# Optimization experiments

Hardware: AMD Instinct MI355X
Metric: run time of the kernel (lower is better)

## Reference

```python
import jax, jax.numpy as jnp
import numpy as np

B = 1024      # batch
HG = 28       # grid side (28x28 image -> graph)
N = HG * HG   # 784 nodes per sample
K = 70        # node_sampled (relaxed categorical classes)
GCN_OUT = 48
H_DIM = 400
Z = 70
IMG = 784
TEMP = 0.5


def _grid_edges():
    idx = np.arange(N).reshape(HG, HG)
    src = np.concatenate([idx[:, :-1].ravel(), idx[:, 1:].ravel(), idx[:-1, :].ravel(), idx[1:, :].ravel()])
    dst = np.concatenate([idx[:, 1:].ravel(), idx[:, :-1].ravel(), idx[1:, :].ravel(), idx[:-1, :].ravel()])
    loop = np.arange(N)
    return (np.concatenate([src, loop]).astype(np.int32),
            np.concatenate([dst, loop]).astype(np.int32))


def _lin(key, fi, fo):
    kw, kb = jax.random.split(key)
    s = 1.0 / np.sqrt(fi)
    return (jax.random.uniform(kw, (fi, fo), jnp.float32, -s, s),
            jax.random.uniform(kb, (fo,), jnp.float32, -s, s))


def setup_inputs() -> dict:
    key = jax.random.key(0)
    ks = jax.random.split(key, 16)
    src, dst = _grid_edges()
    u = jax.random.uniform(ks[2], (B, N, K), jnp.float32, 1e-6, 1.0 - 1e-6)
    inp = {
        'nodes': jax.random.normal(ks[0], (B, N, 2), jnp.float32),
        'logits': jax.random.normal(ks[1], (B, N, K), jnp.float32),
        'gumbel': -jnp.log(-jnp.log(u)),
        'eps': jax.random.normal(ks[3], (B, Z), jnp.float32),
    }
    inp['W1'], inp['b1'] = _lin(ks[4], 2, 16)
    inp['W2'], inp['b2'] = _lin(ks[5], 16, 32)
    inp['W3'], inp['b3'] = _lin(ks[6], 32, GCN_OUT)
    inp['We1'], inp['be1'] = _lin(ks[7], K * GCN_OUT, H_DIM)
    inp['We2'], inp['be2'] = _lin(ks[8], H_DIM, H_DIM)
    inp['Wmu'], inp['bmu'] = _lin(ks[9], H_DIM, Z)
    inp['Wvar'], inp['bvar'] = _lin(ks[10], H_DIM, Z)
    inp['Wd1'], inp['bd1'] = _lin(ks[11], Z, H_DIM)
    inp['Wd2'], inp['bd2'] = _lin(ks[12], H_DIM, IMG)
    inp['edge_src'] = jnp.asarray(src)
    inp['edge_dst'] = jnp.asarray(dst)
    return inp


def reference(nodes, logits, gumbel, eps,
              W1, b1, W2, b2, W3, b3,
              We1, be1, We2, be2,
              Wmu, bmu, Wvar, bvar,
              Wd1, bd1, Wd2, bd2,
              edge_src, edge_dst):
    # symmetric GCN normalization with self loops (already in edge list)
    deg = jnp.zeros((N,), nodes.dtype).at[edge_dst].add(1.0)
    dinv = jax.lax.rsqrt(deg)
    norm = dinv[edge_src] * dinv[edge_dst]  # [E]

    def gcn(h, W, b):
        h = h @ W                                   # [B,N,Fout]
        msg = h[:, edge_src] * norm[None, :, None]  # gather + scale, [B,E,Fout]
        return jnp.zeros_like(h).at[:, edge_dst].add(msg) + b

    h = jax.nn.relu(gcn(nodes, W1, b1))
    h = jax.nn.relu(gcn(h, W2, b2))
    h = jax.nn.relu(gcn(h, W3, b3))            # [B,N,48]

    # RelaxedOneHotCategorical(temp=0.5).rsample() == gumbel-softmax
    sample = jax.nn.softmax((logits + gumbel) / TEMP, axis=-1)  # [B,N,K]
    g = jnp.einsum('bnk,bnf->bkf', sample, h).reshape(h.shape[0], K * GCN_OUT)

    # encoder MLP + reparameterize
    e = jax.nn.relu(g @ We1 + be1)
    e = jax.nn.relu(e @ We2 + be2)
    mu = e @ Wmu + bmu
    var = jax.nn.softplus(e @ Wvar + bvar)
    z = mu + eps * jnp.sqrt(var + 1e-10)

    # decoder
    d = jax.nn.relu(z @ Wd1 + bd1)
    x_rec = jax.nn.sigmoid(d @ Wd2 + bd2)      # [B,784]
    return x_rec
```

## Files before the change

### kernel.cpp

```cpp
#include <hip/hip_runtime.h>
#include <hip/hip_bf16.h>


#define BB 1024
#define HG 28
#define NN 784
#define KK 70
#define F3 48
#define HD 400
#define ZD 70
#define IMGD 784

typedef __hip_bfloat16 bf16;
typedef __attribute__((ext_vector_type(8))) short s8v;
typedef __attribute__((ext_vector_type(4))) float f32x4;

__device__ __forceinline__ float dinv_ij(int i, int j){
  int deg = 1 + (i>0) + (i<HG-1) + (j>0) + (j<HG-1);
  return rsqrtf((float)deg);
}

__device__ __forceinline__ unsigned pk2(float a, float b){
  union { bf16 h; unsigned short u; } ua, ub;
  ua.h = __float2bfloat16(a); ub.h = __float2bfloat16(b);
  return ((unsigned)ub.u << 16) | ua.u;
}

__device__ __forceinline__ short bfbits(float v){
  union { bf16 h; short s; } u; u.h = __float2bfloat16(v); return u.s;
}

#define SYNC_LDS() do {                                   \
    asm volatile("" ::: "memory");                        \
    asm volatile("s_waitcnt lgkmcnt(0)" ::: "memory");    \
    __builtin_amdgcn_s_barrier();                         \
    asm volatile("" ::: "memory");                        \
  } while(0)

__global__ __launch_bounds__(256, 2)
void gcn_fused(const float* __restrict__ nodes,
               const float* __restrict__ W1, const float* __restrict__ b1,
               const float* __restrict__ W2, const float* __restrict__ b2,
               const float* __restrict__ W3, const float* __restrict__ b3,
               bf16* __restrict__ h3){
  __shared__ __align__(16) char smem[73216];
  float* regA = (float*)smem;
  float* regB = (float*)(smem + 36288);
  float* wbuf = (float*)(smem + 64512);
  float* W1s = wbuf;          float* b1s = wbuf + 32;
  float* W2s = wbuf + 48;     float* b2s = wbuf + 560;
  float* W3s = wbuf + 592;    float* b3s = wbuf + 2128;

  int tid = threadIdx.x;
  if (tid < 32)  W1s[tid] = W1[tid];
  if (tid < 16)  b1s[tid] = b1[tid];
  for (int t = tid; t < 512;  t += 256) W2s[t] = W2[t];
  if (tid < 32)  b2s[tid] = b2[tid];
  for (int t = tid; t < 1536; t += 256) W3s[t] = W3[t];
  if (tid < 48)  b3s[tid] = b3[tid];

  int b = blockIdx.x >> 2, s = blockIdx.x & 3;
  int base3 = s*7;
  int base2 = base3 - 1;
  int base1 = base3 - 2;
  const float* nb = nodes + (size_t)b*NN*2;
  __syncthreads();

  {
    float* h1s = regA;
    for (int t = tid; t < 308; t += 256){
      int lr = t/28, j = t - lr*28;
      int r = base1 + lr;
      float o[16] __attribute__((aligned(16)));
      if (r < 0 || r >= HG){
        #pragma unroll
        for (int f=0; f<16; f++) o[f] = 0.f;
      } else {
        float dn = dinv_ij(r,j);
        float a0 = dn*nb[(r*HG+j)*2+0], a1 = dn*nb[(r*HG+j)*2+1];
        if (r > 0)   { float w=dinv_ij(r-1,j); a0 += w*nb[((r-1)*HG+j)*2]; a1 += w*nb[((r-1)*HG+j)*2+1]; }
        if (r < HG-1){ float w=dinv_ij(r+1,j); a0 += w*nb[((r+1)*HG+j)*2]; a1 += w*nb[((r+1)*HG+j)*2+1]; }
        if (j > 0)   { float w=dinv_ij(r,j-1); a0 += w*nb[(r*HG+j-1)*2];   a1 += w*nb[(r*HG+j-1)*2+1]; }
        if (j < HG-1){ float w=dinv_ij(r,j+1); a0 += w*nb[(r*HG+j+1)*2];   a1 += w*nb[(r*HG+j+1)*2+1]; }
        a0 *= dn; a1 *= dn;
        #pragma unroll
        for (int f=0; f<16; f++) o[f] = fmaxf(a0*W1s[f] + a1*W1s[16+f] + b1s[f], 0.f);
      }
      float* dst = h1s + t*20;
      #pragma unroll
      for (int qq=0; qq<4; qq++) *(float4*)(dst + 4*qq) = *(float4*)&o[4*qq];
    }
  }
  __syncthreads();

  if (tid < 252){
    const float* h1s = regA;
    float* agg1 = regB;
    int lr = tid/28, j = tid - lr*28;
    int r = base2 + lr;
    float o[16] __attribute__((aligned(16)));
    if (r < 0 || r >= HG){
      #pragma unroll
      for (int f=0; f<16; f++) o[f] = 0.f;
    } else {
      int ln = (lr+1)*28 + j;
      float dn = dinv_ij(r,j);
      float wu = dinv_ij(r-1,j), wd = dinv_ij(r+1,j);
      float wl = (j>0)    ? dinv_ij(r,j-1) : 0.f;
      float wr = (j<HG-1) ? dinv_ij(r,j+1) : 0.f;
      const float* pc = h1s + ln*20;
      #pragma unroll
      for (int qq=0; qq<4; qq++){
        float4 vc = *(const float4*)(pc + 4*qq);
        float4 vu = *(const float4*)(pc - 28*20 + 4*qq);
        float4 vd = *(const float4*)(pc + 28*20 + 4*qq);
        float4 vl = *(const float4*)(pc - 20 + 4*qq);
        float4 vr = *(const float4*)(pc + 20 + 4*qq);
        o[4*qq+0] = dn*(dn*vc.x + wu*vu.x + wd*vd.x + wl*vl.x + wr*vr.x);
        o[4*qq+1] = dn*(dn*vc.y + wu*vu.y + wd*vd.y + wl*vl.y + wr*vr.y);
        o[4*qq+2] = dn*(dn*vc.z + wu*vu.z + wd*vd.z + wl*vl.z + wr*vr.z);
        o[4*qq+3] = dn*(dn*vc.w + wu*vu.w + wd*vd.w + wl*vl.w + wr*vr.w);
      }
    }
    float* dst = agg1 + tid*20;
    #pragma unroll
    for (int qq=0; qq<4; qq++) *(float4*)(dst + 4*qq) = *(float4*)&o[4*qq];
  }
  __syncthreads();

  {
    const float* agg1 = regB;
    float* h2s = regA;
    int tx = tid & 7, ty = tid >> 3;
    float4 w2r[16];
    #pragma unroll
    for (int fi=0; fi<16; fi++) w2r[fi] = *(const float4*)&W2s[fi*32 + tx*4];
    float4 bb = *(const float4*)&b2s[tx*4];
    #pragma unroll
    for (int i=0; i<8; i++){
      int n = ty + 32*i;
      if (n < 252){
        float af[16] __attribute__((aligned(16)));
        const float* ap = agg1 + n*20;
        #pragma unroll
        for (int qq=0; qq<4; qq++) *(float4*)&af[4*qq] = *(const float4*)(ap + 4*qq);
        float4 acc = bb;
        #pragma unroll
        for (int fi=0; fi<16; fi++){
          float a = af[fi];
          acc.x += a*w2r[fi].x; acc.y += a*w2r[fi].y;
          acc.z += a*w2r[fi].z; acc.w += a*w2r[fi].w;
        }
        acc.x = fmaxf(acc.x,0.f); acc.y = fmaxf(acc.y,0.f);
        acc.z = fmaxf(acc.z,0.f); acc.w = fmaxf(acc.w,0.f);
        *(float4*)&h2s[n*36 + tx*4] = acc;
      }
    }
  }
  __syncthreads();

  if (tid < 196){
    const float* h2s = regA;
    float* agg2 = regB;
    int lr = tid/28, j = tid - lr*28;
    int r = base3 + lr;
    int ln = (lr+1)*28 + j;
    float dn = dinv_ij(r,j);
    float wu = dinv_ij(r-1,j), wd = dinv_ij(r+1,j);
    float wl = (j>0)    ? dinv_ij(r,j-1) : 0.f;
    float wr = (j<HG-1) ? dinv_ij(r,j+1) : 0.f;
    const float* pc = h2s + ln*36;
    float* dst = agg2 + tid*36;
    #pragma unroll
    for (int qq=0; qq<8; qq++){
      float4 vc = *(const float4*)(pc + 4*qq);
      float4 vu = *(const float4*)(pc - 28*36 + 4*qq);
      float4 vd = *(const float4*)(pc + 28*36 + 4*qq);
      float4 vl = *(const float4*)(pc - 36 + 4*qq);
      float4 vr = *(const float4*)(pc + 36 + 4*qq);
      float4 o;
      o.x = dn*(dn*vc.x + wu*vu.x + wd*vd.x + wl*vl.x + wr*vr.x);
      o.y = dn*(dn*vc.y + wu*vu.y + wd*vd.y + wl*vl.y + wr*vr.y);
      o.z = dn*(dn*vc.z + wu*vu.z + wd*vd.z + wl*vl.z + wr*vr.z);
      o.w = dn*(dn*vc.w + wu*vu.w + wd*vd.w + wl*vl.w + wr*vr.w);
      *(float4*)(dst + 4*qq) = o;
    }
  }
  __syncthreads();

  {
    bf16* h3buf = (bf16*)regA;
    if (tid < 252){
      const float* agg2 = regB;
      int tx = tid % 12, ty = tid / 12;
      float4 w3r[32];
      #pragma unroll
      for (int fi=0; fi<32; fi++) w3r[fi] = *(const float4*)&W3s[fi*48 + tx*4];
      float4 bb = *(const float4*)&b3s[tx*4];
      #pragma unroll
      for (int i=0; i<10; i++){
        int n = ty + 21*i;
        if (n < 196){
          float af[32] __attribute__((aligned(16)));
          const float* ap = agg2 + n*36;
          #pragma unroll
          for (int qq=0; qq<8; qq++) *(float4*)&af[4*qq] = *(const float4*)(ap + 4*qq);
          float4 acc = bb;
          #pragma unroll
          for (int fi=0; fi<32; fi++){
            float a = af[fi];
            acc.x += a*w3r[fi].x; acc.y += a*w3r[fi].y;
            acc.z += a*w3r[fi].z; acc.w += a*w3r[fi].w;
          }
          uint2 pv;
          pv.x = pk2(fmaxf(acc.x,0.f), fmaxf(acc.y,0.f));
          pv.y = pk2(fmaxf(acc.z,0.f), fmaxf(acc.w,0.f));
          *(uint2*)((char*)h3buf + n*112 + tx*8) = pv;
        }
      }
    }
  }
  __syncthreads();

  {
    const char* h3buf = (const char*)regA;
    uint4* dst = (uint4*)(h3 + ((size_t)b*NN + base3*28)*F3);
    for (int t = tid; t < 1176; t += 256){
      int n = t/6, gq = t - n*6;
      dst[t] = *(const uint4*)(h3buf + n*112 + gq*16);
    }
  }
}

__global__ __launch_bounds__(256)
void einsum_mfma_kernel(const float* __restrict__ logits, const float* __restrict__ gumbel,
                        const bf16* __restrict__ h3, float* __restrict__ g){
  __shared__ __align__(16) unsigned smemD[2][7488];
  const int SLO = 2880, HTO = 5760;

  int b = blockIdx.x, tid = threadIdx.x;
  int l = tid & 63, w = tid >> 6;
  int n_loc = tid >> 2, q = tid & 3;
  int kstart = q << 4;
  int kcnt = (q < 3) ? 16 : 22;
  int kc2 = kcnt >> 1;
  int m_pair = tid >> 3;
  int half = (tid >> 2) & 1;
  int ks = w >> 1, mh = w & 1;
  int mtoff = mh ? 3 : 0, mtcnt = mh ? 2 : 3;

  for (int t = tid; t < 720; t += 256){
    int bb = t >= 360, r = t - bb*360;
    smemD[bb][2520 + r] = 0u;
    smemD[bb][SLO + 2520 + r] = 0u;
  }

  f32x4 acc[3][3];
  #pragma unroll
  for (int mt=0; mt<3; mt++)
    #pragma unroll
    for (int bt=0; bt<3; bt++) acc[mt][bt] = (f32x4){0.f,0.f,0.f,0.f};

  float2 lxA[11], gxA[11], lxB[11], gxB[11];
  uint2 hA0A, hB0A, hA1A, hB1A;
  uint2 hA0B, hB0B, hA1B, hB1B;
  int hm0 = tid/12, hj0 = tid - hm0*12;
  int tt1 = tid + 256;
  int hm1 = tt1/12, hj1 = tt1 - hm1*12;

  auto issue_into = [&](int c, float2 (&lx)[11], float2 (&gx)[11],
                        uint2& hA0, uint2& hB0, uint2& hA1, uint2& hB1){
    int c0 = c << 6;
    int node = c0 + n_loc;
    bool v = node < NN;
    const float* lp = logits + ((size_t)b*NN + node)*KK + kstart;
    const float* gp = gumbel + ((size_t)b*NN + node)*KK + kstart;
    int nld = (q < 3) ? 8 : 11;
    #pragma unroll
    for (int s=0; s<11; s++){
      bool a = v && (s < nld);
      lx[s] = a ? *(const float2*)(lp + 2*s) : (float2){0.f,0.f};
      gx[s] = a ? *(const float2*)(gp + 2*s) : (float2){0.f,0.f};
    }
    bool vA0 = (c0 + 2*hm0)     < NN;
    bool vB0 = (c0 + 2*hm0 + 1) < NN;
    const uint2* p0 = (const uint2*)(h3 + ((size_t)b*NN + c0 + 2*hm0)*F3 + 4*hj0);
    hA0 = vA0 ? p0[0]  : (uint2){0u,0u};
    hB0 = vB0 ? p0[12] : (uint2){0u,0u};
    if (tid < 128){
      bool vA1 = (c0 + 2*hm1)     < NN;
      bool vB1 = (c0 + 2*hm1 + 1) < NN;
      const uint2* p1 = (const uint2*)(h3 + ((size_t)b*NN + c0 + 2*hm1)*F3 + 4*hj1);
      hA1 = vA1 ? p1[0]  : (uint2){0u,0u};
      hB1 = vB1 ? p1[12] : (uint2){0u,0u};
    }
  };

  auto consume_from = [&](int c, unsigned* buf, float2 (&lx)[11], float2 (&gx)[11],
                          uint2& hA0, uint2& hB0, uint2& hA1, uint2& hB1){
    int c0 = c << 6;
    bool v = (c0 + n_loc) < NN;
    float x[22];
    #pragma unroll
    for (int s=0; s<11; s++){
      x[2*s]   = 2.f*(lx[s].x + gx[s].x);
      x[2*s+1] = 2.f*(lx[s].y + gx[s].y);
    }
    float mx = -1e30f;
    #pragma unroll
    for (int i=0; i<22; i++) if (i < kcnt) mx = fmaxf(mx, x[i]);
    mx = fmaxf(mx, __shfl_xor(mx, 1));
    mx = fmaxf(mx, __shfl_xor(mx, 2));
    float sum = 0.f;
    #pragma unroll
    for (int i=0; i<22; i++) if (i < kcnt){ x[i] = __expf(x[i]-mx); sum += x[i]; }
    sum += __shfl_xor(sum, 1);
    sum += __shfl_xor(sum, 2);
    float rs = v ? 1.0f/sum : 0.f;
    #pragma unroll
    for (int i=0; i<22; i++){
      if (i < kcnt){
        float p = x[i]*rs;
        unsigned hb = (unsigned)(unsigned short)bfbits(p);
        union { short s; bf16 h; } uh; uh.s = (short)hb;
        float lo = p - __bfloat162float(uh.h);
        unsigned lb = (unsigned)(unsigned short)bfbits(lo);
        unsigned phb = (unsigned)__shfl_xor((int)hb, 4);
        unsigned plb = (unsigned)__shfl_xor((int)lb, 4);
        unsigned dh = (half==0) ? (hb | (phb<<16)) : (phb | (hb<<16));
        unsigned dl = (half==0) ? (lb | (plb<<16)) : (plb | (lb<<16));
        bool doW = (half==0) ? (i < kc2) : (i >= kc2);
        if (doW){
          int k = kstart + i;
          int col = m_pair ^ (((k>>4)&3)<<3);
          buf[k*36 + col] = dh;
          buf[SLO + k*36 + col] = dl;
        }
      }
    }
    {
      unsigned d0 = (hA0.x & 0xFFFFu) | (hB0.x << 16);
      unsigned d1 = (hA0.x >> 16)     | (hB0.x & 0xFFFF0000u);
      unsigned d2 = (hA0.y & 0xFFFFu) | (hB0.y << 16);
      unsigned d3 = (hA0.y >> 16)     | (hB0.y & 0xFFFF0000u);
      #pragma unroll
      for (int i2=0; i2<4; i2++){
        int f = 4*hj0 + i2;
        int col = hm0 ^ (((f>>4)&3)<<3);
        unsigned dv = (i2==0)?d0:(i2==1)?d1:(i2==2)?d2:d3;
        buf[HTO + f*36 + col] = dv;
      }
      if (tid < 128){
        unsigned e0 = (hA1.x & 0xFFFFu) | (hB1.x << 16);
        unsigned e1 = (hA1.x >> 16)     | (hB1.x & 0xFFFF0000u);
        unsigned e2 = (hA1.y & 0xFFFFu) | (hB1.y << 16);
        unsigned e3 = (hA1.y >> 16)     | (hB1.y & 0xFFFF0000u);
        #pragma unroll
        for (int i2=0; i2<4; i2++){
          int f = 4*hj1 + i2;
          int col = hm1 ^ (((f>>4)&3)<<3);
          unsigned dv = (i2==0)?e0:(i2==1)?e1:(i2==2)?e2:e3;
          buf[HTO + f*36 + col] = dv;
        }
      }
    }
  };

  auto mfma_phase = [&](const unsigned* buf){
    int pr = (ks<<4) + ((l>>4)<<2);
    s8v Af[3], Al[3], Bf[3];
    #pragma unroll
    for (int mt=0; mt<3; mt++) if (mt < mtcnt){
      int row = (mtoff+mt)*16 + (l&15);
      int col = pr ^ (((row>>4)&3)<<3);
      Af[mt] = *(const s8v*)&buf[row*36 + col];
      Al[mt] = *(const s8v*)&buf[SLO + row*36 + col];
    }
    #pragma unroll
    for (int bt=0; bt<3; bt++){
      int f = bt*16 + (l&15);
      int col = pr ^ (((f>>4)&3)<<3);
      Bf[bt] = *(const s8v*)&buf[HTO + f*36 + col];
    }
    #pragma unroll
    for (int mt=0; mt<3; mt++) if (mt < mtcnt)
      #pragma unroll
      for (int bt=0; bt<3; bt++){
        acc[mt][bt] = __builtin_amdgcn_mfma_f32_16x16x32_bf16(Af[mt], Bf[bt], acc[mt][bt], 0, 0, 0);
        acc[mt][bt] = __builtin_amdgcn_mfma_f32_16x16x32_bf16(Al[mt], Bf[bt], acc[mt][bt], 0, 0, 0);
      }
  };

  issue_into(0, lxA, gxA, hA0A, hB0A, hA1A, hB1A);
  issue_into(1, lxB, gxB, hA0B, hB0B, hA1B, hB1B);
  consume_from(0, smemD[0], lxA, gxA, hA0A, hB0A, hA1A, hB1A);
  SYNC_LDS();

  for (int c = 0; c < 13; c++){
    if (c + 2 <= 12){
      if ((c & 1) == 0) issue_into(c+2, lxA, gxA, hA0A, hB0A, hA1A, hB1A);
      else              issue_into(c+2, lxB, gxB, hA0B, hB0B, hA1B, hB1B);
    }
    if (c < 12){
      if (((c+1) & 1) == 0) consume_from(c+1, smemD[(c+1)&1], lxA, gxA, hA0A, hB0A, hA1A, hB1A);
      else                  consume_from(c+1, smemD[(c+1)&1], lxB, gxB, hA0B, hB0B, hA1B, hB1B);
    }
    mfma_phase(smemD[c&1]);
    SYNC_LDS();
  }

  float* cred = (float*)&smemD[0][0];
  if (ks == 0){
    #pragma unroll
    for (int mt=0; mt<3; mt++) if (mt < mtcnt)
      #pragma unroll
      for (int bt=0; bt<3; bt++)
        #pragma unroll
        for (int r=0; r<4; r++){
          int row = (mtoff+mt)*16 + (l>>4)*4 + r;
          int col = bt*16 + (l&15);
          cred[row*49 + col] = acc[mt][bt][r];
        }
  }
  __syncthreads();
  if (ks == 1){
    #pragma unroll
    for (int mt=0; mt<3; mt++) if (mt < mtcnt)
      #pragma unroll
      for (int bt=0; bt<3; bt++)
        #pragma unroll
        for (int r=0; r<4; r++){
          int row = (mtoff+mt)*16 + (l>>4)*4 + r;
          int col = bt*16 + (l&15);
          cred[row*49 + col] += acc[mt][bt][r];
        }
  }
  __syncthreads();
  for (int t = tid; t < KK*F3; t += 256){
    int r = t / F3, c2 = t - r*F3;
    g[(size_t)b*(KK*F3) + t] = cred[r*49 + c2];
  }
}

template<int ACT>
__global__ __launch_bounds__(256)
void dense_kernel(const float* __restrict__ A, const float* __restrict__ W,
                  const float* __restrict__ bias, float* __restrict__ out,
                  int M, int K, int Nn, int kChunk){
  __shared__ float As[16][65];
  __shared__ float Bs[16][64];
  int tx = threadIdx.x & 15, ty = threadIdx.x >> 4;
  int m0 = blockIdx.x*64, n0 = blockIdx.y*64;
  int ks = blockIdx.z * kChunk;
  int ke = min(K, ks + kChunk);
  int a_kk = threadIdx.x & 15, a_mm = threadIdx.x >> 4;
  int b_nn = threadIdx.x & 63, b_k0 = threadIdx.x >> 6;
  float ra[4], rb[4];
  float acc[4][4] = {};

  #pragma unroll
  for (int s=0; s<4; s++){
    int gk = ks + a_kk;
    ra[s] = (gk < ke) ? A[(size_t)(m0 + a_mm + s*16)*K + gk] : 0.f;
  }
  #pragma unroll
  for (int s=0; s<4; s++){
    int gk = ks + b_k0 + s*4, gn = n0 + b_nn;
    rb[s] = (gk < ke && gn < Nn) ? W[(size_t)gk*Nn + gn] : 0.f;
  }

  for (int k0 = ks; k0 < ke; k0 += 16){
    #pragma unroll
    for (int s=0; s<4; s++) As[a_kk][a_mm + s*16] = ra[s];
    #pragma unroll
    for (int s=0; s<4; s++) Bs[b_k0 + s*4][b_nn] = rb[s];
    __syncthreads();
    if (k0 + 16 < ke){
      #pragma unroll
      for (int s=0; s<4; s++){
        int gk = k0 + 16 + a_kk;
        ra[s] = (gk < ke) ? A[(size_t)(m0 + a_mm + s*16)*K + gk] : 0.f;
      }
      #pragma unroll
      for (int s=0; s<4; s++){
        int gk = k0 + 16 + b_k0 + s*4, gn = n0 + b_nn;
        rb[s] = (gk < ke && gn < Nn) ? W[(size_t)gk*Nn + gn] : 0.f;
      }
    }
    #pragma unroll
    for (int kk=0; kk<16; kk++){
      float a[4], bv[4];
      #pragma unroll
      for (int i2=0; i2<4; i2++) a[i2] = As[kk][ty*4+i2];
      #pragma unroll
      for (int j2=0; j2<4; j2++) bv[j2] = Bs[kk][tx*4+j2];
      #pragma unroll
      for (int i2=0; i2<4; i2++)
        #pragma unroll
        for (int j2=0; j2<4; j2++) acc[i2][j2] += a[i2]*bv[j2];
    }
    __syncthreads();
  }

  if (ACT == 2){
    float* po = out + (size_t)blockIdx.z*M*Nn;
    #pragma unroll
    for (int j2=0; j2<4; j2++){
      int gn = n0 + tx*4 + j2;
      if (gn < Nn){
        #pragma unroll
        for (int i2=0; i2<4; i2++)
          po[(size_t)(m0 + ty*4 + i2)*Nn + gn] = acc[i2][j2];
      }
    }
  } else {
    #pragma unroll
    for (int j2=0; j2<4; j2++){
      int gn = n0 + tx*4 + j2;
      if (gn < Nn){
        float bb = bias[gn];
        #pragma unroll
        for (int i2=0; i2<4; i2++){
          float v = acc[i2][j2] + bb;
          v = (ACT == 0) ? fmaxf(v, 0.f) : 1.0f/(1.0f + __expf(-v));
          out[(size_t)(m0 + ty*4 + i2)*Nn + gn] = v;
        }
      }
    }
  }
}

__global__ __launch_bounds__(256)
void dense_dualB_partial(const float* __restrict__ A, const float* __restrict__ Wmu,
                         const float* __restrict__ Wvar, float* __restrict__ out,
                         int M, int K, int Nn, int kChunk){
  __shared__ float As[16][65];
  __shared__ float Bs[16][64];
  int tx = threadIdx.x & 15, ty = threadIdx.x >> 4;
  int m0 = blockIdx.x*64, n0 = blockIdx.y*64;
  int ks = blockIdx.z * kChunk;
  int ke = min(K, ks + kChunk);
  int a_kk = threadIdx.x & 15, a_mm = threadIdx.x >> 4;
  int b_nn = threadIdx.x & 63, b_k0 = threadIdx.x >> 6;
  float ra[4], rb[4];
  float acc[4][4] = {};

  auto bload = [&](int gk, int gn)->float{
    if (gk >= ke || gn >= Nn) return 0.f;
    return (gn < ZD) ? Wmu[(size_t)gk*ZD + gn] : Wvar[(size_t)gk*ZD + gn - ZD];
  };

  #pragma unroll
  for (int s=0; s<4; s++){
    int gk = ks + a_kk;
    ra[s] = (gk < ke) ? A[(size_t)(m0 + a_mm + s*16)*K + gk] : 0.f;
  }
  #pragma unroll
  for (int s=0; s<4; s++) rb[s] = bload(ks + b_k0 + s*4, n0 + b_nn);

  for (int k0 = ks; k0 < ke; k0 += 16){
    #pragma unroll
    for (int s=0; s<4; s++) As[a_kk][a_mm + s*16] = ra[s];
    #pragma unroll
    for (int s=0; s<4; s++) Bs[b_k0 + s*4][b_nn] = rb[s];
    __syncthreads();
    if (k0 + 16 < ke){
      #pragma unroll
      for (int s=0; s<4; s++){
        int gk = k0 + 16 + a_kk;
        ra[s] = (gk < ke) ? A[(size_t)(m0 + a_mm + s*16)*K + gk] : 0.f;
      }
      #pragma unroll
      for (int s=0; s<4; s++) rb[s] = bload(k0 + 16 + b_k0 + s*4, n0 + b_nn);
    }
    #pragma unroll
    for (int kk=0; kk<16; kk++){
      float a[4], bv[4];
      #pragma unroll
      for (int i2=0; i2<4; i2++) a[i2] = As[kk][ty*4+i2];
      #pragma unroll
      for (int j2=0; j2<4; j2++) bv[j2] = Bs[kk][tx*4+j2];
      #pragma unroll
      for (int i2=0; i2<4; i2++)
        #pragma unroll
        for (int j2=0; j2<4; j2++) acc[i2][j2] += a[i2]*bv[j2];
    }
    __syncthreads();
  }

  float* po = out + (size_t)blockIdx.z*M*Nn;
  #pragma unroll
  for (int j2=0; j2<4; j2++){
    int gn = n0 + tx*4 + j2;
    if (gn < Nn){
      #pragma unroll
      for (int i2=0; i2<4; i2++)
        po[(size_t)(m0 + ty*4 + i2)*Nn + gn] = acc[i2][j2];
    }
  }
}

template<int ACT>
__global__ __launch_bounds__(256)
void reduce_bias_act(const float* __restrict__ part, const float* __restrict__ bias,
                     float* __restrict__ out, int M, int Nn, int S){
  int idx = blockIdx.x*256 + threadIdx.x;
  if (idx >= M*Nn) return;
  int n = idx % Nn;
  float s = bias[n];
  for (int i=0; i<S; i++) s += part[(size_t)i*M*Nn + idx];
  out[idx] = (ACT == 0) ? fmaxf(s, 0.f) : 1.0f/(1.0f + __expf(-s));
}

__global__ __launch_bounds__(256)
void reduce_reparam(const float* __restrict__ part, const float* __restrict__ bmu,
                    const float* __restrict__ bvar, const float* __restrict__ eps,
                    float* __restrict__ z, int S){
  int idx = blockIdx.x*256 + threadIdx.x;
  int b = idx / ZD, zi = idx - b*ZD;
  float mu = bmu[zi], va = bvar[zi];
  for (int s=0; s<S; s++){
    const float* pr = part + ((size_t)s*BB + b)*140;
    mu += pr[zi];
    va += pr[ZD + zi];
  }
  float sp = fmaxf(va, 0.f) + log1pf(__expf(-fabsf(va)));
  z[idx] = mu + eps[idx]*sqrtf(sp + 1e-10f);
}

extern "C" void kernel_launch(void* const* d_in, const int* in_sizes, int n_in,
                              void* d_out, int out_size, void* d_ws, size_t ws_size,
                              hipStream_t stream){
  (void)in_sizes; (void)n_in; (void)out_size; (void)ws_size;
  const float* nodes  = (const float*)d_in[0];
  const float* logits = (const float*)d_in[1];
  const float* gumbel = (const float*)d_in[2];
  const float* eps    = (const float*)d_in[3];
  const float* W1 =(const float*)d_in[4],  *b1 =(const float*)d_in[5];
  const float* W2 =(const float*)d_in[6],  *b2 =(const float*)d_in[7];
  const float* W3 =(const float*)d_in[8],  *b3 =(const float*)d_in[9];
  const float* We1=(const float*)d_in[10], *be1=(const float*)d_in[11];
  const float* We2=(const float*)d_in[12], *be2=(const float*)d_in[13];
  const float* Wmu=(const float*)d_in[14], *bmu=(const float*)d_in[15];
  const float* Wvr=(const float*)d_in[16], *bvr=(const float*)d_in[17];
  const float* Wd1=(const float*)d_in[18], *bd1=(const float*)d_in[19];
  const float* Wd2=(const float*)d_in[20], *bd2=(const float*)d_in[21];

  char* ws = (char*)d_ws;
  bf16*  h3 = (bf16*)(ws);
  float* g  = (float*)(ws + 77070336);
  float* e1 = (float*)(ws + 90832896);
  float* e2 = (float*)(ws + 92471296);
  float* zb = (float*)(ws + 94109696);
  float* dd = (float*)(ws + 94396416);
  float* part = (float*)(ws);
  float* out = (float*)d_out;

  gcn_fused<<<4096, 256, 0, stream>>>(nodes, W1, b1, W2, b2, W3, b3, h3);
  einsum_mfma_kernel<<<1024, 256, 0, stream>>>(logits, gumbel, h3, g);
  dense_kernel<2><<<dim3(16, 7, 8), 256, 0, stream>>>(g, We1, nullptr, part, 1024, 3360, 400, 432);
  reduce_bias_act<0><<<1600, 256, 0, stream>>>(part, be1, e1, 1024, 400, 8);
  dense_kernel<2><<<dim3(16, 7, 4), 256, 0, stream>>>(e1, We2, nullptr, part, 1024, 400, 400, 112);
  reduce_bias_act<0><<<1600, 256, 0, stream>>>(part, be2, e2, 1024, 400, 4);
  dense_dualB_partial<<<dim3(16, 3, 4), 256, 0, stream>>>(e2, Wmu, Wvr, part, 1024, 400, 140, 112);
  reduce_reparam<<<280, 256, 0, stream>>>(part, bmu, bvr, eps, zb, 4);
  dense_kernel<0><<<dim3(16, 7, 1), 256, 0, stream>>>(zb, Wd1, bd1, dd, 1024, 70, 400, 70);
  dense_kernel<2><<<dim3(16, 13, 4), 256, 0, stream>>>(dd, Wd2, nullptr, part, 1024, 400, 784, 112);
  reduce_bias_act<1><<<3136, 256, 0, stream>>>(part, bd2, out, 1024, 784, 4);
}
```

Measured before the change: 410.0 us.

## Single-buffer einsum LDS and register prefetch to raise occupancy

The einsum kernel goes from double-buffered shared memory and two sets of register prefetch buffers to one LDS buffer and one register set. It adds a second barrier per chunk and sets launch bounds to target 5 blocks per CU. The aim is to cut LDS and VGPR use so more blocks stay resident and hide latency. In exchange, the overlap inside each block is reduced: loads are prefetched only one chunk ahead and packing no longer overlaps MFMA.

```diff
diff --git a/kernel.cpp b/kernel.cpp
--- a/kernel.cpp
+++ b/kernel.cpp
@@ -232,10 +232,10 @@
   }
 }
 
-__global__ __launch_bounds__(256)
+__global__ __launch_bounds__(256, 5)
 void einsum_mfma_kernel(const float* __restrict__ logits, const float* __restrict__ gumbel,
                         const bf16* __restrict__ h3, float* __restrict__ g){
-  __shared__ __align__(16) unsigned smemD[2][7488];
+  __shared__ __align__(16) unsigned smemS[7488];
   const int SLO = 2880, HTO = 5760;
 
   int b = blockIdx.x, tid = threadIdx.x;
@@ -250,9 +250,9 @@
   int mtoff = mh ? 3 : 0, mtcnt = mh ? 2 : 3;
 
   for (int t = tid; t < 720; t += 256){
-    int bb = t >= 360, r = t - bb*360;
-    smemD[bb][2520 + r] = 0u;
-    smemD[bb][SLO + 2520 + r] = 0u;
+    int bb2 = t >= 360, r = t - bb2*360;
+    if (bb2) smemS[SLO + 2520 + r] = 0u;
+    else     smemS[2520 + r] = 0u;
   }
 
   f32x4 acc[3][3];
@@ -261,15 +261,13 @@
     #pragma unroll
     for (int bt=0; bt<3; bt++) acc[mt][bt] = (f32x4){0.f,0.f,0.f,0.f};
 
-  float2 lxA[11], gxA[11], lxB[11], gxB[11];
-  uint2 hA0A, hB0A, hA1A, hB1A;
-  uint2 hA0B, hB0B, hA1B, hB1B;
+  float2 lx[11], gx[11];
+  uint2 hA0, hB0, hA1, hB1;
   int hm0 = tid/12, hj0 = tid - hm0*12;
   int tt1 = tid + 256;
   int hm1 = tt1/12, hj1 = tt1 - hm1*12;
 
-  auto issue_into = [&](int c, float2 (&lx)[11], float2 (&gx)[11],
-                        uint2& hA0, uint2& hB0, uint2& hA1, uint2& hB1){
+  auto issue_into = [&](int c){
     int c0 = c << 6;
     int node = c0 + n_loc;
     bool v = node < NN;
@@ -296,8 +294,7 @@
     }
   };
 
-  auto consume_from = [&](int c, unsigned* buf, float2 (&lx)[11], float2 (&gx)[11],
-                          uint2& hA0, uint2& hB0, uint2& hA1, uint2& hB1){
+  auto consume_pack = [&](int c){
     int c0 = c << 6;
     bool v = (c0 + n_loc) < NN;
     float x[22];
@@ -333,8 +330,8 @@
         if (doW){
           int k = kstart + i;
           int col = m_pair ^ (((k>>4)&3)<<3);
-          buf[k*36 + col] = dh;
-          buf[SLO + k*36 + col] = dl;
+          smemS[k*36 + col] = dh;
+          smemS[SLO + k*36 + col] = dl;
         }
       }
     }
@@ -348,7 +345,7 @@
         int f = 4*hj0 + i2;
         int col = hm0 ^ (((f>>4)&3)<<3);
         unsigned dv = (i2==0)?d0:(i2==1)?d1:(i2==2)?d2:d3;
-        buf[HTO + f*36 + col] = dv;
+        smemS[HTO + f*36 + col] = dv;
       }
       if (tid < 128){
         unsigned e0 = (hA1.x & 0xFFFFu) | (hB1.x << 16);
@@ -360,27 +357,27 @@
           int f = 4*hj1 + i2;
           int col = hm1 ^ (((f>>4)&3)<<3);
           unsigned dv = (i2==0)?e0:(i2==1)?e1:(i2==2)?e2:e3;
-          buf[HTO + f*36 + col] = dv;
+          smemS[HTO + f*36 + col] = dv;
         }
       }
     }
   };
 
-  auto mfma_phase = [&](const unsigned* buf){
+  auto mfma_phase = [&](){
     int pr = (ks<<4) + ((l>>4)<<2);
     s8v Af[3], Al[3], Bf[3];
     #pragma unroll
     for (int mt=0; mt<3; mt++) if (mt < mtcnt){
       int row = (mtoff+mt)*16 + (l&15);
       int col = pr ^ (((row>>4)&3)<<3);
-      Af[mt] = *(const s8v*)&buf[row*36 + col];
-      Al[mt] = *(const s8v*)&buf[SLO + row*36 + col];
+      Af[mt] = *(const s8v*)&smemS[row*36 + col];
+      Al[mt] = *(const s8v*)&smemS[SLO + row*36 + col];
     }
     #pragma unroll
     for (int bt=0; bt<3; bt++){
       int f = bt*16 + (l&15);
       int col = pr ^ (((f>>4)&3)<<3);
-      Bf[bt] = *(const s8v*)&buf[HTO + f*36 + col];
+      Bf[bt] = *(const s8v*)&smemS[HTO + f*36 + col];
     }
     #pragma unroll
     for (int mt=0; mt<3; mt++) if (mt < mtcnt)
@@ -391,25 +388,23 @@
       }
   };
 
-  issue_into(0, lxA, gxA, hA0A, hB0A, hA1A, hB1A);
-  issue_into(1, lxB, gxB, hA0B, hB0B, hA1B, hB1B);
-  consume_from(0, smemD[0], lxA, gxA, hA0A, hB0A, hA1A, hB1A);
+  issue_into(0);
+  consume_pack(0);
+  issue_into(1);
   SYNC_LDS();
 
   for (int c = 0; c < 13; c++){
-    if (c + 2 <= 12){
-      if ((c & 1) == 0) issue_into(c+2, lxA, gxA, hA0A, hB0A, hA1A, hB1A);
-      else              issue_into(c+2, lxB, gxB, hA0B, hB0B, hA1B, hB1B);
-    }
+    mfma_phase();
     if (c < 12){
-      if (((c+1) & 1) == 0) consume_from(c+1, smemD[(c+1)&1], lxA, gxA, hA0A, hB0A, hA1A, hB1A);
-      else                  consume_from(c+1, smemD[(c+1)&1], lxB, gxB, hA0B, hB0B, hA1B, hB1B);
-    }
-    mfma_phase(smemD[c&1]);
-    SYNC_LDS();
-  }
-
-  float* cred = (float*)&smemD[0][0];
+      SYNC_LDS();
+      consume_pack(c+1);
+      if (c + 2 <= 12) issue_into(c+2);
+      SYNC_LDS();
+    }
+  }
+
+  __syncthreads();
+  float* cred = (float*)&smemS[0];
   if (ks == 0){
     #pragma unroll
     for (int mt=0; mt<3; mt++) if (mt < mtcnt)
```

New measurement: 582.8 us. 42.2% more time.
